# Optimization experiments

Measured on AMD Instinct MI355X. Metric: run time of the kernel, lower is better.

The kernel has to match this reference:

```python
import jax, jax.numpy as jnp
import numpy as np

B, T, C, KQ = 4096, 128, 20, 100
SCALE = 1.0 / np.sqrt(128.0)  # 1/sqrt(input_length)


def setup_inputs() -> dict:
    key = jax.random.key(0)
    ks = jax.random.split(key, 4)
    x = jax.random.normal(ks[0], (B, T, C), dtype=jnp.float32)
    Wk = jax.random.normal(ks[1], (C, KQ), dtype=jnp.float32) * (1.0 / np.sqrt(C))
    Wq = jax.random.normal(ks[2], (C, KQ), dtype=jnp.float32) * (1.0 / np.sqrt(C))
    Wv = jax.random.normal(ks[3], (C, C), dtype=jnp.float32) * (1.0 / np.sqrt(C))
    bk = jnp.zeros((KQ,), dtype=jnp.float32)
    bq = jnp.zeros((KQ,), dtype=jnp.float32)
    bv = jnp.zeros((C,), dtype=jnp.float32)
    return {"x": x, "Wk": Wk, "bk": bk, "Wq": Wq, "bq": bq, "Wv": Wv, "bv": bv}


def reference(x, Wk, bk, Wq, bq, Wv, bv):
    # Dropout layers are identity at inference.
    k = jax.nn.elu(jnp.einsum('btc,ck->btk', x, Wk) + bk)   # [B,T,KQ]
    q = jax.nn.elu(jnp.einsum('btc,ck->btk', x, Wq) + bq)   # [B,T,KQ]
    v = jnp.tanh(jnp.einsum('btc,cd->btd', x, Wv) + bv)      # [B,T,C]
    # batch_dot(k, q^T): scores[b, i, j] = sum_d k[b,i,d] * q[b,j,d]
    w = jnp.einsum('bid,bjd->bij', k, q) * SCALE              # [B,T,T]
    # Keras Softmax(axis=1): normalize over the first seq axis (rows)
    w = jax.nn.softmax(w, axis=1)
    y = jnp.einsum('bij,bjd->bid', w, v) + x                  # [B,T,C]
    return y
```

## Files before the change

kernel.cpp:

```cpp
#include <hip/hip_runtime.h>
#include <hip/hip_bf16.h>

#define T 128
#define C 20
#define KQ 100
#define NT 256
#define SCALE 0.08838834764831845f
#define K2E   0.12751744f
#define LOG2E 1.4426950408889634f
#define TWOL2E 2.885390081777927f
#define LDS8 136

typedef float  f32x4  __attribute__((ext_vector_type(4)));
typedef short  bf16x8 __attribute__((ext_vector_type(8)));
typedef unsigned int uint32;

__device__ __forceinline__ float exp2i(float x) { return __builtin_amdgcn_exp2f(x); }
__device__ __forceinline__ float rcpi(float x)  { return __builtin_amdgcn_rcpf(x); }

__device__ __forceinline__ short f2bf(float f) {
    unsigned u = __builtin_bit_cast(unsigned, f);
    unsigned r = (u + 0x7FFFu + ((u >> 16) & 1u)) >> 16;
    return (short)r;
}
__device__ __forceinline__ uint32 pk2(float a, float b) {
    __hip_bfloat162 h = __float22bfloat162_rn(float2{a, b});
    uint32 r;
    __builtin_memcpy(&r, &h, 4);
    return r;
}
__device__ __forceinline__ int pkfp8x4(float a, float b, float c, float d) {
    int r = __builtin_amdgcn_cvt_pk_fp8_f32(a, b, 0, false);
    r = __builtin_amdgcn_cvt_pk_fp8_f32(c, d, r, true);
    return r;
}
__device__ __forceinline__ unsigned char fp8_1(float a) {
    return (unsigned char)(__builtin_amdgcn_cvt_pk_fp8_f32(a, 0.f, 0, false) & 0xff);
}

__global__ void prep(const float* __restrict__ Wk, const float* __restrict__ bk,
                     const float* __restrict__ Wq, const float* __restrict__ bq,
                     const float* __restrict__ Wv, const float* __restrict__ bv,
                     short* __restrict__ wkT, short* __restrict__ wqT,
                     short* __restrict__ wvT)
{
    const int t = blockIdx.x * blockDim.x + threadIdx.x;
    if (t < 112 * 32) {
        const int n = t >> 5, c = t & 31;
        float vk = 0.f, vq = 0.f;
        if (n < KQ) {
            if (c < C)       { vk = Wk[c * KQ + n]; vq = Wq[c * KQ + n]; }
            else if (c == C) { vk = bk[n];          vq = bq[n]; }
        }
        wkT[t] = f2bf(vk);
        wqT[t] = f2bf(vq);
        if (t < 32 * 32) {
            const int n2 = t >> 5, c2 = t & 31;
            float vv = 0.f;
            if (n2 < C) {
                if (c2 < C)       vv = Wv[c2 * C + n2] * TWOL2E;
                else if (c2 == C) vv = bv[n2] * TWOL2E;
            }
            wvT[t] = f2bf(vv);
        }
    }
}

__global__ __launch_bounds__(NT, 4) void sa_fused(
    const float* __restrict__ x,
    const short* __restrict__ wAll,
    float* __restrict__ y)
{
    __shared__ __align__(16) unsigned char kp8[T * LDS8];
    __shared__ __align__(16) unsigned char q8 [T * LDS8];
    __shared__ __align__(16) unsigned char vT8[32 * LDS8];

    const int tid  = threadIdx.x;
    const int lane = tid & 63;
    const int w    = __builtin_amdgcn_readfirstlane(tid >> 6);
    const int quad = lane >> 4;
    const int l16  = lane & 15;
    const int b    = blockIdx.x;
    const float* xb = x + (size_t)b * (T * C);

    float4 fA[2], fB[2];
    #pragma unroll
    for (int h = 0; h < 2; ++h) {
        const float* xr = xb + ((w + 4 * h) * 16 + l16) * C;
        fA[h] = (float4){0.f, 0.f, 0.f, 0.f};
        fB[h] = (float4){0.f, 0.f, 0.f, 0.f};
        if (quad < 2) {
            fA[h] = *(const float4*)(xr + quad * 8);
            fB[h] = *(const float4*)(xr + quad * 8 + 4);
        } else if (quad == 2) {
            fA[h] = *(const float4*)(xr + 16);
        }
    }

    {
        const uint4 z4 = {0u, 0u, 0u, 0u};
        unsigned char* pb = (tid < T) ? kp8 : q8;
        *(uint4*)&pb[(tid & (T - 1)) * LDS8 + 112] = z4;
    }

    bf16x8 xf[2];
    #pragma unroll
    for (int h = 0; h < 2; ++h) {
        uint32 p0 = 0, p1 = 0, p2 = 0, p3 = 0;
        if (quad < 2) {
            p0 = pk2(fA[h].x, fA[h].y); p1 = pk2(fA[h].z, fA[h].w);
            p2 = pk2(fB[h].x, fB[h].y); p3 = pk2(fB[h].z, fB[h].w);
        } else if (quad == 2) {
            p0 = pk2(fA[h].x, fA[h].y); p1 = pk2(fA[h].z, fA[h].w);
            p2 = pk2(1.f, 0.f);
        }
        uint4 u4; u4.x = p0; u4.y = p1; u4.z = p2; u4.w = p3;
        xf[h] = __builtin_bit_cast(bf16x8, u4);
    }

    #pragma unroll
    for (int grp = 0; grp < 4; ++grp) {
        bf16x8 wfr[4];
        #pragma unroll
        for (int t = 0; t < 4; ++t)
            wfr[t] = *(const bf16x8*)(wAll + ((grp * 4 + t) * 16 + l16) * 32 + quad * 8);
        #pragma unroll
        for (int s = 0; s < 4; ++s) {
            const int tt = grp * 4 + s;
            #pragma unroll
            for (int h = 0; h < 2; ++h) {
                const int row = (w + 4 * h) * 16 + l16;
                const f32x4 cc = __builtin_amdgcn_mfma_f32_16x16x32_bf16(
                    wfr[s], xf[h], (f32x4){0.f, 0.f, 0.f, 0.f}, 0, 0, 0);
                if (tt < 14) {
                    float e[4];
                    #pragma unroll
                    for (int r = 0; r < 4; ++r) {
                        const float z = cc[r];
                        e[r] = __builtin_amdgcn_fmed3f(z, exp2i(z * LOG2E) - 1.f, 0.f);
                    }
                    unsigned char* dst = (tt < 7)
                        ? &kp8[row * LDS8 + tt * 16 + quad * 4]
                        : &q8 [row * LDS8 + (tt - 7) * 16 + quad * 4];
                    *(int*)dst = pkfp8x4(e[0], e[1], e[2], e[3]);
                } else {
                    #pragma unroll
                    for (int r = 0; r < 4; ++r) {
                        const float e2 = exp2i(cc[r]);
                        vT8[((tt - 14) * 16 + quad * 4 + r) * LDS8 + row]
                            = fp8_1(fmaf(-2.f, rcpi(e2 + 1.f), 1.f));
                    }
                }
            }
        }
    }
    __syncthreads();

    f32x4 acc[2][8];
    #pragma unroll
    for (int h = 0; h < 2; ++h)
        #pragma unroll
        for (int nt = 0; nt < 8; ++nt) acc[h][nt] = (f32x4){0.f, 0.f, 0.f, 0.f};
    __builtin_amdgcn_s_setprio(1);
    #pragma unroll
    for (int ks = 0; ks < 4; ++ks) {
        const long a0 = *(const long*)&q8[( w      * 16 + l16) * LDS8 + ks * 32 + quad * 8];
        const long a1 = *(const long*)&q8[((w + 4) * 16 + l16) * LDS8 + ks * 32 + quad * 8];
        #pragma unroll
        for (int nt = 0; nt < 8; ++nt) {
            const long bk8 = *(const long*)&kp8[(nt * 16 + l16) * LDS8 + ks * 32 + quad * 8];
            acc[0][nt] = __builtin_amdgcn_mfma_f32_16x16x32_fp8_fp8(a0, bk8, acc[0][nt], 0, 0, 0);
            acc[1][nt] = __builtin_amdgcn_mfma_f32_16x16x32_fp8_fp8(a1, bk8, acc[1][nt], 0, 0, 0);
        }
    }
    __builtin_amdgcn_s_setprio(0);

    float ssum[2][4];
    #pragma unroll
    for (int h = 0; h < 2; ++h) {
        #pragma unroll
        for (int r = 0; r < 4; ++r) ssum[h][r] = 0.f;
        #pragma unroll
        for (int nt = 0; nt < 8; ++nt)
            #pragma unroll
            for (int r = 0; r < 4; ++r) {
                const float e = exp2i(acc[h][nt][r] * K2E);
                acc[h][nt][r] = e;
                ssum[h][r] += e;
            }
        #pragma unroll
        for (int r = 0; r < 4; ++r) {
            float s = ssum[h][r];
            s += __shfl_xor(s, 1); s += __shfl_xor(s, 2);
            s += __shfl_xor(s, 4); s += __shfl_xor(s, 8);
            ssum[h][r] = 64.f * rcpi(s);
        }
    }
    __syncthreads();

    #pragma unroll
    for (int nt = 0; nt < 8; ++nt) {
        *(int*)&kp8[(nt * 16 + l16) * LDS8 + w * 16 + quad * 4]
            = pkfp8x4(acc[0][nt][0] * ssum[0][0], acc[0][nt][1] * ssum[0][1],
                      acc[0][nt][2] * ssum[0][2], acc[0][nt][3] * ssum[0][3]);
        *(int*)&kp8[(nt * 16 + l16) * LDS8 + (w + 4) * 16 + quad * 4]
            = pkfp8x4(acc[1][nt][0] * ssum[1][0], acc[1][nt][1] * ssum[1][1],
                      acc[1][nt][2] * ssum[1][2], acc[1][nt][3] * ssum[1][3]);
    }
    __syncthreads();

    f32x4 yacc[2][2];
    #pragma unroll
    for (int h = 0; h < 2; ++h) {
        yacc[h][0] = (f32x4){0.f, 0.f, 0.f, 0.f};
        yacc[h][1] = (f32x4){0.f, 0.f, 0.f, 0.f};
    }
    __builtin_amdgcn_s_setprio(1);
    #pragma unroll
    for (int ks = 0; ks < 4; ++ks) {
        const long a0 = *(const long*)&kp8[( w      * 16 + l16) * LDS8 + ks * 32 + quad * 8];
        const long a1 = *(const long*)&kp8[((w + 4) * 16 + l16) * LDS8 + ks * 32 + quad * 8];
        #pragma unroll
        for (int nt = 0; nt < 2; ++nt) {
            const long bv8 = *(const long*)&vT8[(nt * 16 + l16) * LDS8 + ks * 32 + quad * 8];
            yacc[0][nt] = __builtin_amdgcn_mfma_f32_16x16x32_fp8_fp8(a0, bv8, yacc[0][nt], 0, 0, 0);
            yacc[1][nt] = __builtin_amdgcn_mfma_f32_16x16x32_fp8_fp8(a1, bv8, yacc[1][nt], 0, 0, 0);
        }
    }
    __builtin_amdgcn_s_setprio(0);

    {
        float* yb = y + (size_t)b * (T * C);
        const float inv64 = 1.f / 64.f;
        #pragma unroll
        for (int h = 0; h < 2; ++h)
            #pragma unroll
            for (int r = 0; r < 4; ++r) {
                const int row  = (w + 4 * h) * 16 + quad * 4 + r;
                const int base = row * C;
                yb[base + l16] = yacc[h][0][r] * inv64 + xb[base + l16];
                if (l16 < 4)
                    yb[base + 16 + l16] = yacc[h][1][r] * inv64 + xb[base + 16 + l16];
            }
    }
}

extern "C" void kernel_launch(void* const* d_in, const int* in_sizes, int n_in,
                              void* d_out, int out_size, void* d_ws, size_t ws_size,
                              hipStream_t stream) {
    const float* x  = (const float*)d_in[0];
    const float* Wk = (const float*)d_in[1];
    const float* bk = (const float*)d_in[2];
    const float* Wq = (const float*)d_in[3];
    const float* bq = (const float*)d_in[4];
    const float* Wv = (const float*)d_in[5];
    const float* bv = (const float*)d_in[6];
    float* y = (float*)d_out;

    char* ws = (char*)d_ws;
    short* wkT = (short*)ws;
    short* wqT = (short*)(ws + 7168);
    short* wvT = (short*)(ws + 14336);

    prep<<<14, 256, 0, stream>>>(Wk, bk, Wq, bq, Wv, bv, wkT, wqT, wvT);

    const int B = in_sizes[0] / (T * C);
    sa_fused<<<B, NT, 0, stream>>>(x, (const short*)ws, y);
}
```

Measured before the change: 144.0 us.

## Permute fp8 LDS layout so MFMA operand fetches use 16-byte reads

Reorders the fp8 K/Q/P tiles in shared memory so each lane's two k-slices sit next to each other. Each lane then feeds two MFMAs from one 128-bit LDS load instead of two 64-bit loads, with a row stride of 144 chosen to limit bank conflicts. It also shrinks the V-transpose buffer to 20 rows and skips computing padded V columns. The index permutation must stay consistent across every writer and reader, and the wider stride uses a little more LDS.

New measurement: 147.0 us. 2.1% more time.

```diff
diff --git a/kernel.cpp b/kernel.cpp
--- a/kernel.cpp
+++ b/kernel.cpp
@@ -9,10 +9,12 @@
 #define K2E   0.12751744f
 #define LOG2E 1.4426950408889634f
 #define TWOL2E 2.885390081777927f
-#define LDS8 136
+#define KST 144
+#define VST 136
 
 typedef float  f32x4  __attribute__((ext_vector_type(4)));
 typedef short  bf16x8 __attribute__((ext_vector_type(8)));
+typedef long   lg2    __attribute__((ext_vector_type(2)));
 typedef unsigned int uint32;
 
 __device__ __forceinline__ float exp2i(float x) { return __builtin_amdgcn_exp2f(x); }
@@ -71,9 +73,9 @@
     const short* __restrict__ wAll,
     float* __restrict__ y)
 {
-    __shared__ __align__(16) unsigned char kp8[T * LDS8];
-    __shared__ __align__(16) unsigned char q8 [T * LDS8];
-    __shared__ __align__(16) unsigned char vT8[32 * LDS8];
+    __shared__ __align__(16) unsigned char kp8[T * KST];
+    __shared__ __align__(16) unsigned char q8 [T * KST];
+    __shared__ __align__(16) unsigned char vT8[20 * VST];
 
     const int tid  = threadIdx.x;
     const int lane = tid & 63;
@@ -82,6 +84,7 @@
     const int l16  = lane & 15;
     const int b    = blockIdx.x;
     const float* xb = x + (size_t)b * (T * C);
+    const int qhi  = (quad >> 1) * 32 + (quad & 1) * 4;
 
     float4 fA[2], fB[2];
     #pragma unroll
@@ -98,9 +101,11 @@
     }
 
     {
-        const uint4 z4 = {0u, 0u, 0u, 0u};
+        const uint2 z = {0u, 0u};
         unsigned char* pb = (tid < T) ? kp8 : q8;
-        *(uint4*)&pb[(tid & (T - 1)) * LDS8 + 112] = z4;
+        const int prow = tid & (T - 1);
+        *(uint2*)&pb[prow * KST + 88]  = z;
+        *(uint2*)&pb[prow * KST + 120] = z;
     }
 
     bf16x8 xf[2];
@@ -139,16 +144,20 @@
                         const float z = cc[r];
                         e[r] = __builtin_amdgcn_fmed3f(z, exp2i(z * LOG2E) - 1.f, 0.f);
                     }
+                    const int ct = (tt < 7) ? tt : tt - 7;
+                    const int pbase = (ct & 1) * 64 + (ct >> 1) * 8 + qhi;
                     unsigned char* dst = (tt < 7)
-                        ? &kp8[row * LDS8 + tt * 16 + quad * 4]
-                        : &q8 [row * LDS8 + (tt - 7) * 16 + quad * 4];
+                        ? &kp8[row * KST + pbase]
+                        : &q8 [row * KST + pbase];
                     *(int*)dst = pkfp8x4(e[0], e[1], e[2], e[3]);
                 } else {
-                    #pragma unroll
-                    for (int r = 0; r < 4; ++r) {
-                        const float e2 = exp2i(cc[r]);
-                        vT8[((tt - 14) * 16 + quad * 4 + r) * LDS8 + row]
-                            = fp8_1(fmaf(-2.f, rcpi(e2 + 1.f), 1.f));
+                    if (tt == 14 || quad == 0) {
+                        #pragma unroll
+                        for (int r = 0; r < 4; ++r) {
+                            const float e2 = exp2i(cc[r]);
+                            vT8[((tt - 14) * 16 + quad * 4 + r) * VST + row]
+                                = fp8_1(fmaf(-2.f, rcpi(e2 + 1.f), 1.f));
+                        }
                     }
                 }
             }
@@ -163,14 +172,19 @@
         for (int nt = 0; nt < 8; ++nt) acc[h][nt] = (f32x4){0.f, 0.f, 0.f, 0.f};
     __builtin_amdgcn_s_setprio(1);
     #pragma unroll
-    for (int ks = 0; ks < 4; ++ks) {
-        const long a0 = *(const long*)&q8[( w      * 16 + l16) * LDS8 + ks * 32 + quad * 8];
-        const long a1 = *(const long*)&q8[((w + 4) * 16 + l16) * LDS8 + ks * 32 + quad * 8];
+    for (int kp = 0; kp < 2; ++kp) {
+        const lg2 a0 = __builtin_bit_cast(lg2,
+            *(const uint4*)&q8[( w      * 16 + l16) * KST + quad * 32 + kp * 16]);
+        const lg2 a1 = __builtin_bit_cast(lg2,
+            *(const uint4*)&q8[((w + 4) * 16 + l16) * KST + quad * 32 + kp * 16]);
         #pragma unroll
         for (int nt = 0; nt < 8; ++nt) {
-            const long bk8 = *(const long*)&kp8[(nt * 16 + l16) * LDS8 + ks * 32 + quad * 8];
-            acc[0][nt] = __builtin_amdgcn_mfma_f32_16x16x32_fp8_fp8(a0, bk8, acc[0][nt], 0, 0, 0);
-            acc[1][nt] = __builtin_amdgcn_mfma_f32_16x16x32_fp8_fp8(a1, bk8, acc[1][nt], 0, 0, 0);
+            const lg2 bb = __builtin_bit_cast(lg2,
+                *(const uint4*)&kp8[(nt * 16 + l16) * KST + quad * 32 + kp * 16]);
+            acc[0][nt] = __builtin_amdgcn_mfma_f32_16x16x32_fp8_fp8(a0.x, bb.x, acc[0][nt], 0, 0, 0);
+            acc[0][nt] = __builtin_amdgcn_mfma_f32_16x16x32_fp8_fp8(a0.y, bb.y, acc[0][nt], 0, 0, 0);
+            acc[1][nt] = __builtin_amdgcn_mfma_f32_16x16x32_fp8_fp8(a1.x, bb.x, acc[1][nt], 0, 0, 0);
+            acc[1][nt] = __builtin_amdgcn_mfma_f32_16x16x32_fp8_fp8(a1.y, bb.y, acc[1][nt], 0, 0, 0);
         }
     }
     __builtin_amdgcn_s_setprio(0);
@@ -198,12 +212,13 @@
     }
     __syncthreads();
 
+    const int pw0 = (w & 1) * 64 + (w >> 1) * 8 + qhi;
     #pragma unroll
     for (int nt = 0; nt < 8; ++nt) {
-        *(int*)&kp8[(nt * 16 + l16) * LDS8 + w * 16 + quad * 4]
+        *(int*)&kp8[(nt * 16 + l16) * KST + pw0]
             = pkfp8x4(acc[0][nt][0] * ssum[0][0], acc[0][nt][1] * ssum[0][1],
                       acc[0][nt][2] * ssum[0][2], acc[0][nt][3] * ssum[0][3]);
-        *(int*)&kp8[(nt * 16 + l16) * LDS8 + (w + 4) * 16 + quad * 4]
+        *(int*)&kp8[(nt * 16 + l16) * KST + pw0 + 16]
             = pkfp8x4(acc[1][nt][0] * ssum[1][0], acc[1][nt][1] * ssum[1][1],
                       acc[1][nt][2] * ssum[1][2], acc[1][nt][3] * ssum[1][3]);
     }
@@ -215,16 +230,23 @@
         yacc[h][0] = (f32x4){0.f, 0.f, 0.f, 0.f};
         yacc[h][1] = (f32x4){0.f, 0.f, 0.f, 0.f};
     }
+    const int vr1 = (l16 < 4) ? 16 + l16 : l16;
     __builtin_amdgcn_s_setprio(1);
     #pragma unroll
-    for (int ks = 0; ks < 4; ++ks) {
-        const long a0 = *(const long*)&kp8[( w      * 16 + l16) * LDS8 + ks * 32 + quad * 8];
-        const long a1 = *(const long*)&kp8[((w + 4) * 16 + l16) * LDS8 + ks * 32 + quad * 8];
+    for (int kp = 0; kp < 2; ++kp) {
+        const lg2 a0 = __builtin_bit_cast(lg2,
+            *(const uint4*)&kp8[( w      * 16 + l16) * KST + quad * 32 + kp * 16]);
+        const lg2 a1 = __builtin_bit_cast(lg2,
+            *(const uint4*)&kp8[((w + 4) * 16 + l16) * KST + quad * 32 + kp * 16]);
         #pragma unroll
         for (int nt = 0; nt < 2; ++nt) {
-            const long bv8 = *(const long*)&vT8[(nt * 16 + l16) * LDS8 + ks * 32 + quad * 8];
-            yacc[0][nt] = __builtin_amdgcn_mfma_f32_16x16x32_fp8_fp8(a0, bv8, yacc[0][nt], 0, 0, 0);
-            yacc[1][nt] = __builtin_amdgcn_mfma_f32_16x16x32_fp8_fp8(a1, bv8, yacc[1][nt], 0, 0, 0);
+            const int rowv = nt ? vr1 : l16;
+            const long b0 = *(const long*)&vT8[rowv * VST + (kp * 2    ) * 32 + quad * 8];
+            const long b1 = *(const long*)&vT8[rowv * VST + (kp * 2 + 1) * 32 + quad * 8];
+            yacc[0][nt] = __builtin_amdgcn_mfma_f32_16x16x32_fp8_fp8(a0.x, b0, yacc[0][nt], 0, 0, 0);
+            yacc[0][nt] = __builtin_amdgcn_mfma_f32_16x16x32_fp8_fp8(a0.y, b1, yacc[0][nt], 0, 0, 0);
+            yacc[1][nt] = __builtin_amdgcn_mfma_f32_16x16x32_fp8_fp8(a1.x, b0, yacc[1][nt], 0, 0, 0);
+            yacc[1][nt] = __builtin_amdgcn_mfma_f32_16x16x32_fp8_fp8(a1.y, b1, yacc[1][nt], 0, 0, 0);
         }
     }
     __builtin_amdgcn_s_setprio(0);
```
